# Kernel optimization log

Measured on AMD Instinct MI355X. Metric: run time of the kernel, lower is better.

## Reference

```python
import jax, jax.numpy as jnp
import numpy as np

B, F, T = 2, 512, 512
D, N, H = 1024, 16, 64   # hidden, heads, head_dim
K = 32                   # time-bias MLP kernal_size
FILT = 4096              # FFN filter size
L = 4                    # num_decoder_blocks
EPS = 1e-6


def _glorot(key, shape, fan_in, fan_out):
    lim = np.sqrt(6.0 / (fan_in + fan_out)).astype(np.float32)
    return jax.random.uniform(key, shape, jnp.float32, -lim, lim)


def setup_inputs() -> dict:
    key = jax.random.key(0)
    ks = jax.random.split(key, 18)
    inp = {
        'decoder_inputs': jax.random.normal(ks[0], (B, F, D), jnp.float32),
        'encoder_outputs': jax.random.normal(ks[1], (B, T, D), jnp.float32),
        'decoder_times_dist': jax.random.uniform(ks[2], (B, F, F), jnp.float32),
        'decoder_encoder_times_dist': jax.random.uniform(ks[3], (B, F, T), jnp.float32),
        'dec_self_attn_bias': jnp.zeros((B, 1, 1, F), jnp.float32),
        'enc_dec_attn_bias': jnp.zeros((B, 1, 1, T), jnp.float32),
        # per-block stacked parameters (leading dim L)
        'Wq': _glorot(ks[4], (L, D, N, H), D, D),
        'Wk': _glorot(ks[5], (L, D, N, H), D, D),
        'Wv': _glorot(ks[6], (L, D, N, H), D, D),
        'Wo': _glorot(ks[7], (L, N, H, D), D, D),
        'Wth': _glorot(ks[8], (L, 1, K), 1, K),
        'bth': jnp.zeros((L, K), jnp.float32),
        'Wto': _glorot(ks[9], (L, K, 1), K, 1),
        'bto': jnp.zeros((L, 1), jnp.float32),
        'Wf1': _glorot(ks[10], (L, D, FILT), D, FILT),
        'bf1': jnp.zeros((L, FILT), jnp.float32),
        'Wf2': _glorot(ks[11], (L, FILT, D), FILT, D),
        'bf2': jnp.zeros((L, D), jnp.float32),
    }
    return inp


def _norm(x):
    # non-trainable LayerNormalization: (x - mean) / (std + eps)
    m = jnp.mean(x, axis=-1, keepdims=True)
    s = jnp.sqrt(jnp.mean((x - m) ** 2, axis=-1, keepdims=True))
    return (x - m) / (s + EPS)


def _attention(x, src, dist, bias, Wq, Wk, Wv, Wo, Wth, bth, Wto, bto):
    q = jnp.einsum('bfd,dnh->bfnh', x, Wq) * (H ** -0.5)
    k = jnp.einsum('btd,dnh->btnh', src, Wk)
    v = jnp.einsum('btd,dnh->btnh', src, Wv)
    # learned time bias: [B,F,T,1] -> relu MLP(K) -> 1 -> [B,F,T]
    hbias = jax.nn.relu(dist[..., None] @ Wth + bth)        # [B,F,T,K]
    qs_bias = (hbias @ Wto + bto)[..., 0]                   # [B,F,T]
    logits = jnp.einsum('btnh,bfnh->bnft', k, q)            # [B,N,F,T]
    logits = logits + bias + qs_bias[:, None]
    w = jax.nn.softmax(logits, axis=-1)
    out = jnp.einsum('bnft,btnh->bfnh', w, v)
    return jnp.einsum('bfnh,nhd->bfd', out, Wo)


def reference(decoder_inputs, encoder_outputs, decoder_times_dist,
              decoder_encoder_times_dist, dec_self_attn_bias, enc_dec_attn_bias,
              Wq, Wk, Wv, Wo, Wth, bth, Wto, bto, Wf1, bf1, Wf2, bf2):
    # decoder_times_dist / dec_self_attn_bias are accepted but unused (as in source call)
    x = decoder_inputs
    for i in range(L):
        # enc-dec attention with pre-norm + residual
        y = _attention(_norm(x), encoder_outputs, decoder_encoder_times_dist,
                       enc_dec_attn_bias, Wq[i], Wk[i], Wv[i], Wo[i],
                       Wth[i], bth[i], Wto[i], bto[i])
        x = x + y
        # FFN with pre-norm + residual
        y = jax.nn.relu(_norm(x) @ Wf1[i] + bf1[i]) @ Wf2[i] + bf2[i]
        x = x + y
    return _norm(x)
```

## Files before the change

kernel.cpp:

```cpp
#include <hip/hip_runtime.h>

typedef unsigned short u16;
typedef __attribute__((ext_vector_type(8))) unsigned short u16x8;
typedef __attribute__((ext_vector_type(4))) unsigned short u16x4;
typedef __attribute__((ext_vector_type(4))) float f32x4;

#define DEVI __device__ __forceinline__

DEVI u16 f2bf(float f){
  unsigned u = __float_as_uint(f);
  u += 0x7FFFu + ((u >> 16) & 1u);
  return (u16)(u >> 16);
}

DEVI void gload16(const void* g, void* l){
  __builtin_amdgcn_global_load_lds((const __attribute__((address_space(1))) void*)g,
                                   (__attribute__((address_space(3))) void*)l, 16, 0, 0);
}

DEVI float wave_sum(float v){
#pragma unroll
  for (int o = 32; o; o >>= 1) v += __shfl_xor(v, o, 64);
  return v;
}

#define MFMA16(a,b,c) __builtin_amdgcn_mfma_f32_16x16x32_bf16((a),(b),(c),0,0,0)

__global__ __launch_bounds__(256) void prep_k(
    const float* __restrict__ Wq, const float* __restrict__ Wk,
    const float* __restrict__ Wv, const float* __restrict__ Wo,
    const float* __restrict__ Wf1, const float* __restrict__ Wf2,
    const float* __restrict__ enc,
    u16* __restrict__ Wqt, u16* __restrict__ Wkt,
    u16* __restrict__ Wvt, u16* __restrict__ Wot,
    u16* __restrict__ Wf1t, u16* __restrict__ Wf2t,
    u16* __restrict__ encb){
  __shared__ u16 tile[32][33];
  const int t = blockIdx.x;
  if (t >= 49152){
    const int i = (t - 49152) * 256 + threadIdx.x;
    float4 v = ((const float4*)enc)[i];
    u16x4 o = { f2bf(v.x), f2bf(v.y), f2bf(v.z), f2bf(v.w) };
    ((u16x4*)encb)[i] = o;
    return;
  }
  const float* in; u16* out; int C, R, r0, c0;
  if (t < 16384){
    const int mat = t >> 10, ti = t & 1023, sel = mat >> 2, l = mat & 3;
    in  = (sel == 0 ? Wq : sel == 1 ? Wk : sel == 2 ? Wv : Wo) + (size_t)l * 1048576;
    out = (sel == 0 ? Wqt : sel == 1 ? Wkt : sel == 2 ? Wvt : Wot) + (size_t)l * 1048576;
    R = 1024; C = 1024; r0 = (ti >> 5) * 32; c0 = (ti & 31) * 32;
  } else if (t < 32768){
    const int t2 = t - 16384, mat = t2 >> 12, ti = t2 & 4095;
    in = Wf1 + (size_t)mat * 4194304; out = Wf1t + (size_t)mat * 4194304;
    R = 1024; C = 4096; r0 = (ti >> 7) * 32; c0 = (ti & 127) * 32;
  } else {
    const int t2 = t - 32768, mat = t2 >> 12, ti = t2 & 4095;
    in = Wf2 + (size_t)mat * 4194304; out = Wf2t + (size_t)mat * 4194304;
    R = 4096; C = 1024; r0 = (ti >> 5) * 32; c0 = (ti & 31) * 32;
  }
  const int tx = threadIdx.x & 31, ty = threadIdx.x >> 5;
#pragma unroll
  for (int k = 0; k < 4; k++)
    tile[ty + k*8][tx] = f2bf(in[(size_t)(r0 + ty + k*8) * C + c0 + tx]);
  __syncthreads();
#pragma unroll
  for (int k = 0; k < 4; k++)
    out[(size_t)(c0 + ty + k*8) * R + r0 + tx] = tile[tx][ty + k*8];
}

__global__ __launch_bounds__(256) void layernorm_k(const float* __restrict__ in, u16* __restrict__ outp){
  const int row = blockIdx.x;
  const int tid = threadIdx.x;
  const float4 v = ((const float4*)(in + (size_t)row * 1024))[tid];
  __shared__ float sb[8];
  const int wid = tid >> 6, lane = tid & 63;
  float s = wave_sum(v.x + v.y + v.z + v.w);
  if (lane == 0) sb[wid] = s;
  __syncthreads();
  const float mean = (sb[0] + sb[1] + sb[2] + sb[3]) * (1.0f / 1024.0f);
  const float dx = v.x - mean, dy = v.y - mean, dz = v.z - mean, dw = v.w - mean;
  float q = wave_sum(dx*dx + dy*dy + dz*dz + dw*dw);
  if (lane == 0) sb[4 + wid] = q;
  __syncthreads();
  const float sd = sqrtf((sb[4] + sb[5] + sb[6] + sb[7]) * (1.0f / 1024.0f));
  const float inv = 1.0f / (sd + 1e-6f);
  u16x4 o = { f2bf(dx*inv), f2bf(dy*inv), f2bf(dz*inv), f2bf(dw*inv) };
  ((u16x4*)outp)[(size_t)row * 256 + tid] = o;
}

__global__ __launch_bounds__(256) void qsbias_k(const float* __restrict__ dist,
    const float* __restrict__ Wth0, const float* __restrict__ bth0,
    const float* __restrict__ Wto0, const float* __restrict__ bto0,
    float* __restrict__ qs0){
  const int ly = blockIdx.y;
  const float* Wth = Wth0 + ly*32;
  const float* bth = bth0 + ly*32;
  const float* Wto = Wto0 + ly*32;
  float* qs = qs0 + (size_t)ly * 524288;
  const int idx = blockIdx.x * 256 + threadIdx.x;
  float4 s4 = ((const float4*)dist)[idx];
  float sv[4] = { s4.x, s4.y, s4.z, s4.w };
  float r[4];
  const float b0 = bto0[ly];
#pragma unroll
  for (int c = 0; c < 4; c++) r[c] = b0;
#pragma unroll
  for (int k = 0; k < 32; k++){
    const float wk = Wth[k], bk = bth[k], ok = Wto[k];
#pragma unroll
    for (int c = 0; c < 4; c++){
      float h = fmaxf(sv[c] * wk + bk, 0.0f);
      r[c] += h * ok;
    }
  }
  ((float4*)qs)[idx] = make_float4(r[0], r[1], r[2], r[3]);
}

template<int MODE, int BN>
DEVI void gemm128_core(const u16* A, int lda, const u16* Bt, int ldb,
                       int Klen, int Nd, void* Cout,
                       const float* bias, float scale,
                       u16* Als, u16* Bls, int row0, int col0){
  constexpr int WN = BN / 2, FN = BN / 32;
  constexpr int BSZ = BN * 64;
  const int tid = threadIdx.x;
  const int wid = tid >> 6, lane = tid & 63;
  const int wm = wid >> 1, wn = wid & 1;
  const int lrow = lane & 15, g = lane >> 4, e7 = lane & 7;
  f32x4 acc[4][FN] = {};

  const int scol = ((lane & 7) ^ ((lane >> 3) & 7)) * 8;
  const u16* Ag = A + (size_t)(row0 + wid*8 + (lane >> 3)) * lda + scol;
  const u16* Bg = Bt + (size_t)(col0 + wid*8 + (lane >> 3)) * ldb + scol;
  const int dst0 = wid * 512;

  const int nt = Klen >> 6;

#define STAGE128(buf, k0)                                                     \
  {                                                                           \
    _Pragma("unroll")                                                         \
    for (int q = 0; q < 4; q++)                                               \
      gload16(Ag + (size_t)q*32*lda + (k0), Als + (buf)*8192 + dst0 + q*2048);\
    _Pragma("unroll")                                                         \
    for (int q = 0; q < BN/32; q++)                                           \
      gload16(Bg + (size_t)q*32*ldb + (k0), Bls + (buf)*BSZ + dst0 + q*2048); \
  }

  STAGE128(0, 0);
  __syncthreads();

  for (int t = 0; t < nt; t++){
    const int cur = t & 1;
    if (t + 1 < nt) STAGE128(cur ^ 1, (t + 1) << 6);
    const u16* Ab = Als + cur * 8192;
    const u16* Bb = Bls + cur * BSZ;
#pragma unroll
    for (int ks = 0; ks < 2; ks++){
      const int sl = (((ks << 2) + g) ^ e7) << 3;
      u16x8 av[4], bv[FN];
#pragma unroll
      for (int mi = 0; mi < 4; mi++)
        av[mi] = *(const u16x8*)(Ab + (wm*64 + mi*16 + lrow) * 64 + sl);
#pragma unroll
      for (int ni = 0; ni < FN; ni++)
        bv[ni] = *(const u16x8*)(Bb + (wn*WN + ni*16 + lrow) * 64 + sl);
#pragma unroll
      for (int mi = 0; mi < 4; mi++)
#pragma unroll
        for (int ni = 0; ni < FN; ni++)
          acc[mi][ni] = MFMA16(av[mi], bv[ni], acc[mi][ni]);
    }
    __syncthreads();
  }
#undef STAGE128

#pragma unroll
  for (int mi = 0; mi < 4; mi++){
#pragma unroll
    for (int ni = 0; ni < FN; ni++){
      const int col = col0 + wn*WN + ni*16 + lrow;
#pragma unroll
      for (int j = 0; j < 4; j++){
        const int row = row0 + wm*64 + mi*16 + g*4 + j;
        float v = acc[mi][ni][j];
        if (MODE == 3) v = fmaxf(v + bias[col], 0.0f);
        if (MODE == 0 || MODE == 3)
          ((u16*)Cout)[(size_t)row * Nd + col] = f2bf(v);
        else if (MODE == 6)
          ((u16*)Cout)[(size_t)((col >> 9)*16 + (row >> 6)) * 32768
                       + (row & 63) * 512 + (col & 511)] = f2bf(v);
        else
          ((float*)Cout)[(size_t)row * Nd + col] = v;
      }
    }
  }
}

template<int MODE>
__global__ __launch_bounds__(256) void gemm128_k(const u16* __restrict__ A, int lda,
    const u16* __restrict__ Bt, int ldb, int Klen, int Nd, void* __restrict__ Cout,
    const float* __restrict__ bias, float scale){
  __shared__ __align__(16) u16 Als[2 * 8192];
  __shared__ __align__(16) u16 Bls[2 * 4096];
  gemm128_core<MODE, 64>(A, lda, Bt, ldb, Klen, Nd, Cout, bias, scale,
                         Als, Bls, blockIdx.y * 128, blockIdx.x * 64);
}

__global__ __launch_bounds__(256) void gemmKV_k(const u16* __restrict__ encb,
    const u16* __restrict__ Wkt, const u16* __restrict__ Wvt,
    u16* __restrict__ Kb, u16* __restrict__ Vt){
  __shared__ __align__(16) u16 Als[2 * 8192];
  __shared__ __align__(16) u16 Bls[2 * 4096];
  const int z = blockIdx.z, l = z >> 1;
  if ((z & 1) == 0)
    gemm128_core<0, 64>(encb, 1024, Wkt + (size_t)l*1048576, 1024, 1024, 1024,
                        Kb + (size_t)l*1048576, nullptr, 1.0f,
                        Als, Bls, blockIdx.y * 128, blockIdx.x * 64);
  else
    gemm128_core<6, 64>(Wvt + (size_t)l*1048576, 1024, encb, 1024, 1024, 1024,
                        Vt + (size_t)l*1048576, nullptr, 1.0f,
                        Als, Bls, blockIdx.y * 128, blockIdx.x * 64);
}

__global__ __launch_bounds__(256) void gemm_splitk_k(const u16* __restrict__ A, int lda,
    const u16* __restrict__ Bt, int ldb, int Klen, float* __restrict__ part){
  __shared__ __align__(16) u16 Als[2 * 8192];
  __shared__ __align__(16) u16 Bls[2 * 4096];
  const int z = blockIdx.z;
  gemm128_core<5, 64>(A + (size_t)z * Klen, lda, Bt + (size_t)z * Klen, ldb, Klen, 1024,
                      part + (size_t)z * 1048576, nullptr, 1.0f,
                      Als, Bls, blockIdx.y * 128, blockIdx.x * 64);
}

template<int BIAS, int LAST>
__global__ __launch_bounds__(256) void reduce_ln_k(const float* __restrict__ part,
    const float* __restrict__ bias, float* __restrict__ x, u16* __restrict__ xn,
    float* __restrict__ dout){
  const int row = blockIdx.x, tid = threadIdx.x;
  const size_t idx = (size_t)row * 256 + tid;
  float4 v = ((const float4*)x)[idx];
  float4 p0 = ((const float4*)part)[idx];
  float4 p1 = ((const float4*)(part + 1048576))[idx];
  float4 p2 = ((const float4*)(part + 2097152))[idx];
  float4 p3 = ((const float4*)(part + 3145728))[idx];
  v.x += p0.x + p1.x + p2.x + p3.x;
  v.y += p0.y + p1.y + p2.y + p3.y;
  v.z += p0.z + p1.z + p2.z + p3.z;
  v.w += p0.w + p1.w + p2.w + p3.w;
  if (BIAS){
    const float4 b = *(const float4*)(bias + tid * 4);
    v.x += b.x; v.y += b.y; v.z += b.z; v.w += b.w;
  }
  if (!LAST) ((float4*)x)[idx] = v;

  __shared__ float sb[8];
  const int wid = tid >> 6, lane = tid & 63;
  float s = wave_sum(v.x + v.y + v.z + v.w);
  if (lane == 0) sb[wid] = s;
  __syncthreads();
  const float mean = (sb[0] + sb[1] + sb[2] + sb[3]) * (1.0f / 1024.0f);
  const float dx = v.x - mean, dy = v.y - mean, dz = v.z - mean, dw = v.w - mean;
  float q = wave_sum(dx*dx + dy*dy + dz*dz + dw*dw);
  if (lane == 0) sb[4 + wid] = q;
  __syncthreads();
  const float sd = sqrtf((sb[4] + sb[5] + sb[6] + sb[7]) * (1.0f / 1024.0f));
  const float inv = 1.0f / (sd + 1e-6f);
  if (LAST){
    ((float4*)dout)[idx] = make_float4(dx*inv, dy*inv, dz*inv, dw*inv);
  } else {
    u16x4 o = { f2bf(dx*inv), f2bf(dy*inv), f2bf(dz*inv), f2bf(dw*inv) };
    ((u16x4*)xn)[idx] = o;
  }
}

__global__ __launch_bounds__(256, 1) void attn_k(const u16* __restrict__ xn,
    const u16* __restrict__ Wqt,
    const u16* __restrict__ Kb, const u16* __restrict__ Vt,
    const float* __restrict__ qs, const float* __restrict__ abias,
    u16* __restrict__ aout){
  const int n = blockIdx.x, f0 = blockIdx.y * 64, b = blockIdx.z;
  const int w = threadIdx.x >> 6, lane = threadIdx.x & 63;
  const int l15 = lane & 15, g = lane >> 4, e7 = lane & 7;
  const int fw = f0 + w * 16;
  __shared__ __align__(16) u16 Pl[4][16 * 512];
  u16* pw = &Pl[w][0];

  u16x8 qf0, qf1;
  {
    u16* Als = &Pl[0][0];
    u16* Bls = &Pl[1][0];
    const int wm = w >> 1, wn = w & 1;
    f32x4 qac[2][2] = {};
    const int scol = ((lane & 7) ^ ((lane >> 3) & 7)) * 8;
    const u16* Ag = xn + (size_t)(b*512 + f0 + w*8 + (lane >> 3)) * 1024 + scol;
    const u16* Bg = Wqt + (size_t)(n*64 + w*8 + (lane >> 3)) * 1024 + scol;
    const int dq = w * 512;

#define STAGEQ(buf, k0)                                         \
    gload16(Ag + (k0),            Als + (buf)*4096 + dq);       \
    gload16(Ag + 32*1024 + (k0),  Als + (buf)*4096 + dq + 2048);\
    gload16(Bg + (k0),            Bls + (buf)*4096 + dq);       \
    gload16(Bg + 32*1024 + (k0),  Bls + (buf)*4096 + dq + 2048);

    STAGEQ(0, 0);
    __syncthreads();
    for (int t = 0; t < 16; t++){
      const int cur = t & 1;
      if (t < 15){ STAGEQ(cur ^ 1, (t + 1) << 6); }
      const u16* Ab = Als + cur * 4096;
      const u16* Bb = Bls + cur * 4096;
#pragma unroll
      for (int ks = 0; ks < 2; ks++){
        const int sl = (((ks << 2) + g) ^ e7) << 3;
        u16x8 av[2], bv[2];
#pragma unroll
        for (int mi = 0; mi < 2; mi++)
          av[mi] = *(const u16x8*)(Ab + (wm*32 + mi*16 + l15) * 64 + sl);
#pragma unroll
        for (int ni = 0; ni < 2; ni++)
          bv[ni] = *(const u16x8*)(Bb + (wn*32 + ni*16 + l15) * 64 + sl);
#pragma unroll
        for (int mi = 0; mi < 2; mi++)
#pragma unroll
          for (int ni = 0; ni < 2; ni++)
            qac[mi][ni] = MFMA16(av[mi], bv[ni], qac[mi][ni]);
      }
      __syncthreads();
    }
#undef STAGEQ

    u16* Qt = &Pl[2][0];
#pragma unroll
    for (int mi = 0; mi < 2; mi++)
#pragma unroll
      for (int ni = 0; ni < 2; ni++)
#pragma unroll
        for (int j = 0; j < 4; j++){
          const int r = wm*32 + mi*16 + g*4 + j;
          const int c = wn*32 + ni*16 + l15;
          const int byte = r*128 + (((c >> 3) ^ (r & 7)) << 4) + (c & 7)*2;
          *(u16*)((char*)Qt + byte) = f2bf(qac[mi][ni][j] * 0.125f);
        }
    __syncthreads();
    const int r = w*16 + l15;
    const char* qrow = (char*)Qt + r*128;
    qf0 = *(const u16x8*)(qrow + ((g ^ (r & 7)) << 4));
    qf1 = *(const u16x8*)(qrow + (((4 + g) ^ (r & 7)) << 4));
    __syncthreads();
  }

  f32x4 acc[32];
  const u16* kp = Kb + ((size_t)b*512 + l15) * 1024 + n*64 + g*8;
#pragma unroll
  for (int tf = 0; tf < 32; tf++){
    u16x8 k0 = *(const u16x8*)(kp + (size_t)tf*16*1024);
    u16x8 k1 = *(const u16x8*)(kp + (size_t)tf*16*1024 + 32);
    f32x4 z = {0.f, 0.f, 0.f, 0.f};
    z = MFMA16(k0, qf0, z);
    acc[tf] = MFMA16(k1, qf1, z);
  }

  const float* qsp = qs + ((size_t)b*512 + fw + l15) * 512 + g*4;
  const float* abp = abias + (size_t)b*512 + g*4;
  float m = -3.0e38f;
#pragma unroll
  for (int tf = 0; tf < 32; tf++){
    float4 qv = *(const float4*)(qsp + tf*16);
    float4 av = *(const float4*)(abp + tf*16);
    acc[tf][0] += qv.x + av.x;
    acc[tf][1] += qv.y + av.y;
    acc[tf][2] += qv.z + av.z;
    acc[tf][3] += qv.w + av.w;
    m = fmaxf(m, fmaxf(fmaxf(acc[tf][0], acc[tf][1]), fmaxf(acc[tf][2], acc[tf][3])));
  }
  m = fmaxf(m, __shfl_xor(m, 16, 64));
  m = fmaxf(m, __shfl_xor(m, 32, 64));

  float s = 0.f;
#pragma unroll
  for (int tf = 0; tf < 32; tf++){
#pragma unroll
    for (int j = 0; j < 4; j++){
      float e = __expf(acc[tf][j] - m);
      acc[tf][j] = e; s += e;
    }
  }
  s += __shfl_xor(s, 16, 64);
  s += __shfl_xor(s, 32, 64);
  const float inv = 1.0f / s;
  float invj[4];
#pragma unroll
  for (int j = 0; j < 4; j++) invj[j] = __shfl(inv, g*4 + j, 64);

#pragma unroll
  for (int tf = 0; tf < 32; tf++){
    const int chunk = tf*2 + (g >> 1);
    const int boff = (l15 << 10) + ((chunk ^ e7) << 4) + ((g & 1) << 3);
    u16x4 pk = { f2bf(acc[tf][0]), f2bf(acc[tf][1]), f2bf(acc[tf][2]), f2bf(acc[tf][3]) };
    *(u16x4*)((char*)pw + boff) = pk;
  }

  f32x4 oacc[4] = {};
  const u16* vp = Vt + ((size_t)(b*16 + n)*64 + l15) * 512 + g*8;
  for (int kk = 0; kk < 16; kk++){
    u16x8 pa = *(const u16x8*)((char*)pw + (l15 << 10) + ((((kk << 2) + g) ^ e7) << 4));
#pragma unroll
    for (int nf = 0; nf < 4; nf++){
      u16x8 vb = *(const u16x8*)(vp + (size_t)nf*16*512 + kk*32);
      oacc[nf] = MFMA16(pa, vb, oacc[nf]);
    }
  }

  u16* op = aout + ((size_t)b*512 + fw + g*4) * 1024 + n*64 + l15;
#pragma unroll
  for (int nf = 0; nf < 4; nf++)
#pragma unroll
    for (int j = 0; j < 4; j++)
      op[(size_t)j*1024 + nf*16] = f2bf(oacc[nf][j] * invj[j]);
}

extern "C" void kernel_launch(void* const* d_in, const int* in_sizes, int n_in,
                              void* d_out, int out_size, void* d_ws, size_t ws_size,
                              hipStream_t stream){
  const float* dec_in   = (const float*)d_in[0];
  const float* enc      = (const float*)d_in[1];
  const float* dist     = (const float*)d_in[3];
  const float* abias    = (const float*)d_in[5];
  const float* Wq  = (const float*)d_in[6];
  const float* Wk  = (const float*)d_in[7];
  const float* Wv  = (const float*)d_in[8];
  const float* Wo  = (const float*)d_in[9];
  const float* Wth = (const float*)d_in[10];
  const float* bth = (const float*)d_in[11];
  const float* Wto = (const float*)d_in[12];
  const float* bto = (const float*)d_in[13];
  const float* Wf1 = (const float*)d_in[14];
  const float* bf1 = (const float*)d_in[15];
  const float* Wf2 = (const float*)d_in[16];
  const float* bf2 = (const float*)d_in[17];
  float* dout = (float*)d_out;

  char* wp = (char*)d_ws;
  auto alloc = [&](size_t n) -> char* {
    char* p = wp; wp += (n + 255) & ~(size_t)255; return p;
  };
  float* x     = (float*)alloc((size_t)1048576 * 4);
  u16*  xn     = (u16*)alloc((size_t)1048576 * 2);
  u16*  encb   = (u16*)alloc((size_t)1048576 * 2);
  u16*  Wqt    = (u16*)alloc((size_t)4194304 * 2);
  u16*  Wkt    = (u16*)alloc((size_t)4194304 * 2);
  u16*  Wvt    = (u16*)alloc((size_t)4194304 * 2);
  u16*  Wot    = (u16*)alloc((size_t)4194304 * 2);
  u16*  Wf1t   = (u16*)alloc((size_t)16777216 * 2);
  u16*  Wf2t   = (u16*)alloc((size_t)16777216 * 2);
  u16*  Kb     = (u16*)alloc((size_t)4194304 * 2);
  u16*  Vt     = (u16*)alloc((size_t)4194304 * 2);
  float* qs    = (float*)alloc((size_t)2097152 * 4);
  u16*  aout   = (u16*)alloc((size_t)1048576 * 2);
  u16*  ffh    = (u16*)alloc((size_t)4194304 * 2);
  float* part  = (float*)alloc((size_t)4194304 * 4);

  hipMemcpyAsync(x, dec_in, (size_t)1048576 * 4, hipMemcpyDeviceToDevice, stream);
  prep_k<<<50176, 256, 0, stream>>>(Wq, Wk, Wv, Wo, Wf1, Wf2, enc,
                                    Wqt, Wkt, Wvt, Wot, Wf1t, Wf2t, encb);
  qsbias_k<<<dim3(512, 4), 256, 0, stream>>>(dist, Wth, bth, Wto, bto, qs);
  gemmKV_k<<<dim3(16, 8, 8), 256, 0, stream>>>(encb, Wkt, Wvt, Kb, Vt);
  layernorm_k<<<1024, 256, 0, stream>>>(x, xn);

  for (int i = 0; i < 4; i++){
    const size_t wo = (size_t)i * 1048576;

    attn_k<<<dim3(16, 8, 2), 256, 0, stream>>>(xn, Wqt + wo, Kb + wo, Vt + wo,
                                               qs + (size_t)i * 524288, abias, aout);

    gemm_splitk_k<<<dim3(16, 8, 4), 256, 0, stream>>>(aout, 1024, Wot + wo, 1024, 256, part);
    reduce_ln_k<0, 0><<<1024, 256, 0, stream>>>(part, nullptr, x, xn, nullptr);

    gemm128_k<3><<<dim3(64, 8), 256, 0, stream>>>(xn, 1024, Wf1t + (size_t)i*4194304, 1024,
                                                  1024, 4096, ffh, bf1 + (size_t)i*4096, 1.0f);
    gemm_splitk_k<<<dim3(16, 8, 4), 256, 0, stream>>>(ffh, 4096, Wf2t + (size_t)i*4194304, 4096,
                                                      1024, part);
    if (i < 3)
      reduce_ln_k<1, 0><<<1024, 256, 0, stream>>>(part, bf2 + (size_t)i*1024, x, xn, nullptr);
    else
      reduce_ln_k<1, 1><<<1024, 256, 0, stream>>>(part, bf2 + (size_t)i*1024, x, nullptr, dout);
  }
}
```

Measured before the change: 454.5 us.

## Fuse weight transpose, qs-bias and input copy into fewer launches; raise attn occupancy

The weight transpose/convert kernel now uses 64x64 tiles per block, with each thread loading 16 strided floats and writing 16 contiguous bf16 values as two vector stores, so the LDS staging and barrier are gone. The qs-bias MLP is folded into the same prep launch, the device-to-device copy of the decoder input is folded into the first layernorm, and attn_k's launch bounds allow two blocks per CU. This removes two launches and a memcpy and aims for better write coalescing in the transpose. In exchange, the transpose reads are strided per thread, and the higher attention occupancy target may cap registers and cause spills.

```diff
diff --git a/kernel.cpp b/kernel.cpp
--- a/kernel.cpp
+++ b/kernel.cpp
@@ -30,49 +30,80 @@
     const float* __restrict__ Wq, const float* __restrict__ Wk,
     const float* __restrict__ Wv, const float* __restrict__ Wo,
     const float* __restrict__ Wf1, const float* __restrict__ Wf2,
-    const float* __restrict__ enc,
+    const float* __restrict__ enc, const float* __restrict__ dist,
+    const float* __restrict__ Wth0, const float* __restrict__ bth0,
+    const float* __restrict__ Wto0, const float* __restrict__ bto0,
     u16* __restrict__ Wqt, u16* __restrict__ Wkt,
     u16* __restrict__ Wvt, u16* __restrict__ Wot,
     u16* __restrict__ Wf1t, u16* __restrict__ Wf2t,
-    u16* __restrict__ encb){
-  __shared__ u16 tile[32][33];
+    u16* __restrict__ encb, float* __restrict__ qs0){
   const int t = blockIdx.x;
-  if (t >= 49152){
-    const int i = (t - 49152) * 256 + threadIdx.x;
+  if (t < 12288){
+    const float* in; u16* out; int R, C, r0, c0;
+    if (t < 4096){
+      const int mat = t >> 8, ti = t & 255, sel = mat >> 2, l = mat & 3;
+      in  = (sel == 0 ? Wq : sel == 1 ? Wk : sel == 2 ? Wv : Wo) + (size_t)l * 1048576;
+      out = (sel == 0 ? Wqt : sel == 1 ? Wkt : sel == 2 ? Wvt : Wot) + (size_t)l * 1048576;
+      R = 1024; C = 1024; r0 = (ti >> 4) << 6; c0 = (ti & 15) << 6;
+    } else if (t < 8192){
+      const int t2 = t - 4096, mat = t2 >> 10, ti = t2 & 1023;
+      in = Wf1 + (size_t)mat * 4194304; out = Wf1t + (size_t)mat * 4194304;
+      R = 1024; C = 4096; r0 = (ti >> 6) << 6; c0 = (ti & 63) << 6;
+    } else {
+      const int t2 = t - 8192, mat = t2 >> 10, ti = t2 & 1023;
+      in = Wf2 + (size_t)mat * 4194304; out = Wf2t + (size_t)mat * 4194304;
+      R = 4096; C = 1024; r0 = (ti >> 4) << 6; c0 = (ti & 15) << 6;
+    }
+    const int w = threadIdx.x >> 6, l = threadIdx.x & 63;
+    const float* ip = in + (size_t)(r0 + w*16) * C + c0 + l;
+    float v[16];
+#pragma unroll
+    for (int e = 0; e < 16; e++) v[e] = ip[(size_t)e * C];
+    union { u16x8 v8[2]; u16 e[16]; } ob;
+#pragma unroll
+    for (int e = 0; e < 16; e++) ob.e[e] = f2bf(v[e]);
+    u16* op = out + (size_t)(c0 + l) * R + r0 + w*16;
+    *(u16x8*)op = ob.v8[0];
+    *(u16x8*)(op + 8) = ob.v8[1];
+  } else if (t < 13312){
+    const int i = (t - 12288) * 256 + threadIdx.x;
     float4 v = ((const float4*)enc)[i];
     u16x4 o = { f2bf(v.x), f2bf(v.y), f2bf(v.z), f2bf(v.w) };
     ((u16x4*)encb)[i] = o;
-    return;
-  }
-  const float* in; u16* out; int C, R, r0, c0;
-  if (t < 16384){
-    const int mat = t >> 10, ti = t & 1023, sel = mat >> 2, l = mat & 3;
-    in  = (sel == 0 ? Wq : sel == 1 ? Wk : sel == 2 ? Wv : Wo) + (size_t)l * 1048576;
-    out = (sel == 0 ? Wqt : sel == 1 ? Wkt : sel == 2 ? Wvt : Wot) + (size_t)l * 1048576;
-    R = 1024; C = 1024; r0 = (ti >> 5) * 32; c0 = (ti & 31) * 32;
-  } else if (t < 32768){
-    const int t2 = t - 16384, mat = t2 >> 12, ti = t2 & 4095;
-    in = Wf1 + (size_t)mat * 4194304; out = Wf1t + (size_t)mat * 4194304;
-    R = 1024; C = 4096; r0 = (ti >> 7) * 32; c0 = (ti & 127) * 32;
   } else {
-    const int t2 = t - 32768, mat = t2 >> 12, ti = t2 & 4095;
-    in = Wf2 + (size_t)mat * 4194304; out = Wf2t + (size_t)mat * 4194304;
-    R = 4096; C = 1024; r0 = (ti >> 5) * 32; c0 = (ti & 31) * 32;
-  }
-  const int tx = threadIdx.x & 31, ty = threadIdx.x >> 5;
-#pragma unroll
-  for (int k = 0; k < 4; k++)
-    tile[ty + k*8][tx] = f2bf(in[(size_t)(r0 + ty + k*8) * C + c0 + tx]);
-  __syncthreads();
-#pragma unroll
-  for (int k = 0; k < 4; k++)
-    out[(size_t)(c0 + ty + k*8) * R + r0 + tx] = tile[tx][ty + k*8];
-}
-
-__global__ __launch_bounds__(256) void layernorm_k(const float* __restrict__ in, u16* __restrict__ outp){
+    const int bi = t - 13312, ly = bi >> 9, xi = bi & 511;
+    const float* Wth = Wth0 + ly*32;
+    const float* bth = bth0 + ly*32;
+    const float* Wto = Wto0 + ly*32;
+    float* qs = qs0 + (size_t)ly * 524288;
+    const int idx = xi * 256 + threadIdx.x;
+    float4 s4 = ((const float4*)dist)[idx];
+    float sv[4] = { s4.x, s4.y, s4.z, s4.w };
+    float r[4];
+    const float b0 = bto0[ly];
+#pragma unroll
+    for (int c = 0; c < 4; c++) r[c] = b0;
+#pragma unroll
+    for (int k = 0; k < 32; k++){
+      const float wk = Wth[k], bk = bth[k], ok = Wto[k];
+#pragma unroll
+      for (int c = 0; c < 4; c++){
+        float h = fmaxf(sv[c] * wk + bk, 0.0f);
+        r[c] += h * ok;
+      }
+    }
+    ((float4*)qs)[idx] = make_float4(r[0], r[1], r[2], r[3]);
+  }
+}
+
+template<int COPY>
+__global__ __launch_bounds__(256) void layernorm_k(const float* __restrict__ in,
+                                                   float* __restrict__ x,
+                                                   u16* __restrict__ outp){
   const int row = blockIdx.x;
   const int tid = threadIdx.x;
   const float4 v = ((const float4*)(in + (size_t)row * 1024))[tid];
+  if (COPY) ((float4*)x)[(size_t)row * 256 + tid] = v;
   __shared__ float sb[8];
   const int wid = tid >> 6, lane = tid & 63;
   float s = wave_sum(v.x + v.y + v.z + v.w);
@@ -87,34 +118,6 @@
   const float inv = 1.0f / (sd + 1e-6f);
   u16x4 o = { f2bf(dx*inv), f2bf(dy*inv), f2bf(dz*inv), f2bf(dw*inv) };
   ((u16x4*)outp)[(size_t)row * 256 + tid] = o;
-}
-
-__global__ __launch_bounds__(256) void qsbias_k(const float* __restrict__ dist,
-    const float* __restrict__ Wth0, const float* __restrict__ bth0,
-    const float* __restrict__ Wto0, const float* __restrict__ bto0,
-    float* __restrict__ qs0){
-  const int ly = blockIdx.y;
-  const float* Wth = Wth0 + ly*32;
-  const float* bth = bth0 + ly*32;
-  const float* Wto = Wto0 + ly*32;
-  float* qs = qs0 + (size_t)ly * 524288;
-  const int idx = blockIdx.x * 256 + threadIdx.x;
-  float4 s4 = ((const float4*)dist)[idx];
-  float sv[4] = { s4.x, s4.y, s4.z, s4.w };
-  float r[4];
-  const float b0 = bto0[ly];
-#pragma unroll
-  for (int c = 0; c < 4; c++) r[c] = b0;
-#pragma unroll
-  for (int k = 0; k < 32; k++){
-    const float wk = Wth[k], bk = bth[k], ok = Wto[k];
-#pragma unroll
-    for (int c = 0; c < 4; c++){
-      float h = fmaxf(sv[c] * wk + bk, 0.0f);
-      r[c] += h * ok;
-    }
-  }
-  ((float4*)qs)[idx] = make_float4(r[0], r[1], r[2], r[3]);
 }
 
 template<int MODE, int BN>
@@ -274,7 +277,7 @@
   }
 }
 
-__global__ __launch_bounds__(256, 1) void attn_k(const u16* __restrict__ xn,
+__global__ __launch_bounds__(256, 2) void attn_k(const u16* __restrict__ xn,
     const u16* __restrict__ Wqt,
     const u16* __restrict__ Kb, const u16* __restrict__ Vt,
     const float* __restrict__ qs, const float* __restrict__ abias,
@@ -461,12 +464,11 @@
   u16*  ffh    = (u16*)alloc((size_t)4194304 * 2);
   float* part  = (float*)alloc((size_t)4194304 * 4);
 
-  hipMemcpyAsync(x, dec_in, (size_t)1048576 * 4, hipMemcpyDeviceToDevice, stream);
-  prep_k<<<50176, 256, 0, stream>>>(Wq, Wk, Wv, Wo, Wf1, Wf2, enc,
-                                    Wqt, Wkt, Wvt, Wot, Wf1t, Wf2t, encb);
-  qsbias_k<<<dim3(512, 4), 256, 0, stream>>>(dist, Wth, bth, Wto, bto, qs);
+  prep_k<<<15360, 256, 0, stream>>>(Wq, Wk, Wv, Wo, Wf1, Wf2, enc, dist,
+                                    Wth, bth, Wto, bto,
+                                    Wqt, Wkt, Wvt, Wot, Wf1t, Wf2t, encb, qs);
   gemmKV_k<<<dim3(16, 8, 8), 256, 0, stream>>>(encb, Wkt, Wvt, Kb, Vt);
-  layernorm_k<<<1024, 256, 0, stream>>>(x, xn);
+  layernorm_k<1><<<1024, 256, 0, stream>>>(dec_in, x, xn);
 
   for (int i = 0; i < 4; i++){
     const size_t wo = (size_t)i * 1048576;
```

After: 472.8 us. 1.04x slower.
